# Kernel optimization log

Hardware: AMD Instinct MI355X
Metric: run time of the kernel (lower is better)

Reference implementation:

```python
import jax, jax.numpy as jnp
import numpy as np

B, N, C, H, BS = 4, 4096, 1024, 16, 64
E = C // H          # head dim = 64
EPS = 1e-3

def setup_inputs() -> dict:
    key = jax.random.key(0)
    k0, k1, k2, k3 = jax.random.split(key, 4)
    x = jax.random.normal(k0, (B, N, C), jnp.float32)
    qkv_w = jax.random.normal(k1, (3 * C, C), jnp.float32) * 0.02
    proj_w = jax.random.normal(k2, (C, C), jnp.float32) * 0.02
    proj_b = jax.random.normal(k3, (C,), jnp.float32) * 0.02
    return {"x": x, "qkv_w": qkv_w, "proj_w": proj_w, "proj_b": proj_b}

def reference(x, qkv_w, proj_w, proj_b):
    b, n, c = x.shape
    h, e, bs = H, E, BS
    u = n // bs  # number of buckets
    # qkv projection (no bias), split to (B,H,N,e) per q/k/v
    qkv = (x @ qkv_w.T).reshape(b, n, 3, h, e).transpose(2, 0, 3, 1, 4)
    q, k, v = qkv[0], qkv[1], qkv[2]
    # feature maps: softmax(q) scaled, exp(k)
    q = jax.nn.softmax(q, axis=-1) * (e ** -0.5)
    k = jnp.exp(k)
    # bucket along sequence: (B,H,U,BS,e)
    b_q = q.reshape(b, h, u, bs, e)
    b_k = k.reshape(b, h, u, bs, e)
    b_v = v.reshape(b, h, u, bs, e)
    # per-bucket k sums and inter-bucket cumulative sums
    b_k_cumsum = jnp.cumsum(b_k.sum(axis=-2), axis=-2)            # (B,H,U,e)
    context = jnp.einsum('bhund,bhune->bhude', b_k, b_v)          # (B,H,U,e,e)
    context = jnp.cumsum(context, axis=2)
    # exclusive shift by one bucket (bucket_size > 1 path in original)
    context = jnp.concatenate(
        [jnp.zeros_like(context[:, :, :1]), context[:, :, :-1]], axis=2)
    b_k_cumsum = jnp.concatenate(
        [jnp.zeros_like(b_k_cumsum[:, :, :1]), b_k_cumsum[:, :, :-1]], axis=2)
    # normalizer, clamped from below at eps
    D_inv = 1.0 / jnp.maximum(
        jnp.einsum('bhud,bhund->bhun', b_k_cumsum, b_q), EPS)
    attn = jnp.einsum('bhund,bhude,bhun->bhune', b_q, context, D_inv)
    out = attn.reshape(b, h, n, e).transpose(0, 2, 1, 3).reshape(b, n, c)
    # output projection (dropouts are identity at eval)
    return out @ proj_w.T + proj_b
```

## Files before the change

kernel.cpp:

```cpp
#include <hip/hip_runtime.h>
#include <stdint.h>


typedef unsigned short u16;
typedef u16   u16x4  __attribute__((ext_vector_type(4)));
typedef u16   u16x8  __attribute__((ext_vector_type(8)));
typedef float f32x4  __attribute__((ext_vector_type(4)));
typedef float float4v __attribute__((ext_vector_type(4)));
typedef __bf16 bf16x8 __attribute__((ext_vector_type(8)));

__device__ __forceinline__ u16 f2bf(float f) {
  return __builtin_bit_cast(u16, (__bf16)f);
}
__device__ __forceinline__ float bf2f(u16 h) {
  return (float)__builtin_bit_cast(__bf16, h);
}

__global__ __launch_bounds__(256) void cvt_f32_to_bf16(
    const float* __restrict__ in, u16* __restrict__ out, int n4) {
  int i = blockIdx.x * 256 + threadIdx.x;
  if (i >= n4) return;
  float4v v = reinterpret_cast<const float4v*>(in)[i];
  u16x4 o;
  o.x = f2bf(v.x); o.y = f2bf(v.y); o.z = f2bf(v.z); o.w = f2bf(v.w);
  reinterpret_cast<u16x4*>(out)[i] = o;
}

template <bool BF16_OUT>
__global__ __launch_bounds__(256, 2) void gemm_bt(
    const u16* __restrict__ A,
    const u16* __restrict__ B,
    const float* __restrict__ bias,
    void* __restrict__ Cv,
    int M, int N, int K) {
  __shared__ u16 As[128 * 64];
  __shared__ u16 Bs[128 * 64];
  const int tid  = threadIdx.x;
  const int lane = tid & 63;
  const int wave = tid >> 6;
  const int wm = wave >> 1, wn = wave & 1;
  const int l15 = lane & 15, l4 = lane >> 4;
  const int ntn = N >> 7;
  const int cpx = gridDim.x >> 3;
  const int bid = (blockIdx.x & 7) * cpx + (blockIdx.x >> 3);
  const int bm = bid / ntn, bn = bid % ntn;

  f32x4 acc[4][4] = {};

  const u16* Ab = A + (size_t)(bm * 128) * K;
  const u16* Bb = B + (size_t)(bn * 128) * K;
  const int crow = tid >> 3;
  const int ccol = tid & 7;

  for (int kt = 0; kt < K; kt += 64) {
    u16x8 ra[4], rb[4];
#pragma unroll
    for (int j = 0; j < 4; ++j) {
      int row = crow + 32 * j;
      ra[j] = *reinterpret_cast<const u16x8*>(Ab + (size_t)row * K + kt + ccol * 8);
      rb[j] = *reinterpret_cast<const u16x8*>(Bb + (size_t)row * K + kt + ccol * 8);
    }
    __syncthreads();
#pragma unroll
    for (int j = 0; j < 4; ++j) {
      int row = crow + 32 * j;
      int off = row * 128 + ((ccol * 16) ^ ((row & 7) << 4));
      *reinterpret_cast<u16x8*>(reinterpret_cast<char*>(As) + off) = ra[j];
      *reinterpret_cast<u16x8*>(reinterpret_cast<char*>(Bs) + off) = rb[j];
    }
    __syncthreads();
#pragma unroll
    for (int kk = 0; kk < 2; ++kk) {
      const int cb = kk * 64 + l4 * 16;
      bf16x8 af[4], bfr[4];
#pragma unroll
      for (int mi = 0; mi < 4; ++mi) {
        int row = wm * 64 + mi * 16 + l15;
        af[mi] = *reinterpret_cast<const bf16x8*>(
            reinterpret_cast<const char*>(As) + row * 128 + (cb ^ ((row & 7) << 4)));
      }
#pragma unroll
      for (int ni = 0; ni < 4; ++ni) {
        int row = wn * 64 + ni * 16 + l15;
        bfr[ni] = *reinterpret_cast<const bf16x8*>(
            reinterpret_cast<const char*>(Bs) + row * 128 + (cb ^ ((row & 7) << 4)));
      }
#pragma unroll
      for (int mi = 0; mi < 4; ++mi)
#pragma unroll
        for (int ni = 0; ni < 4; ++ni)
          acc[mi][ni] = __builtin_amdgcn_mfma_f32_16x16x32_bf16(
              af[mi], bfr[ni], acc[mi][ni], 0, 0, 0);
    }
  }

  const int row0 = bm * 128 + wm * 64 + l4 * 4;
  const int col0 = bn * 128 + wn * 64 + l15;
  if constexpr (BF16_OUT) {
    u16* C = (u16*)Cv;
#pragma unroll
    for (int mi = 0; mi < 4; ++mi)
#pragma unroll
      for (int i = 0; i < 4; ++i) {
        size_t r = (size_t)(row0 + mi * 16 + i) * N;
#pragma unroll
        for (int ni = 0; ni < 4; ++ni)
          C[r + col0 + ni * 16] = f2bf(acc[mi][ni][i]);
      }
  } else {
    float* C = (float*)Cv;
    float bv[4];
#pragma unroll
    for (int ni = 0; ni < 4; ++ni) bv[ni] = bias[col0 + ni * 16];
#pragma unroll
    for (int mi = 0; mi < 4; ++mi)
#pragma unroll
      for (int i = 0; i < 4; ++i) {
        size_t r = (size_t)(row0 + mi * 16 + i) * N;
#pragma unroll
        for (int ni = 0; ni < 4; ++ni)
          C[r + col0 + ni * 16] = acc[mi][ni][i] + bv[ni];
      }
  }
}

__global__ __launch_bounds__(256) void featuremap_ctx(
    const u16* __restrict__ qkv,
    u16* __restrict__ Q, u16* __restrict__ ctxb, float* __restrict__ ksum) {
  const int bid = blockIdx.x;
  const int u = bid & 63;
  const int bh = bid >> 6;
  const int b = bh >> 4, h = bh & 15;
  const int tid = threadIdx.x, lane = tid & 63, wave = tid >> 6;
  const int l15 = lane & 15, l4 = lane >> 4;
  __shared__ float ts[64][65];
  __shared__ u16 KtL[64][72];
  __shared__ u16 VtL[64][72];
  __shared__ float dp[64][4];

  const size_t mrow  = (size_t)b * 4096 + u * 64;
  const size_t obase = (size_t)bid * 4096;

#pragma unroll 1
  for (int r = 0; r < 16; ++r) {
    int n = wave * 16 + r;
    float v = bf2f(qkv[(mrow + n) * 3072 + h * 64 + lane]);
    float mx = v;
#pragma unroll
    for (int o = 32; o; o >>= 1) mx = fmaxf(mx, __shfl_xor(mx, o));
    float ex = __expf(v - mx);
    float sm = ex;
#pragma unroll
    for (int o = 32; o; o >>= 1) sm += __shfl_xor(sm, o);
    Q[obase + n * 64 + lane] = f2bf(ex / sm * 0.125f);
  }

  {
    int n = tid >> 2, c = tid & 3;
    const u16* kp = qkv + (mrow + n) * 3072 + 1024 + h * 64 + c * 16;
#pragma unroll
    for (int j = 0; j < 16; ++j) ts[n][c * 16 + j] = __expf(bf2f(kp[j]));
  }
  __syncthreads();
  {
    int d = tid >> 2, c = tid & 3;
    u16x8 o0, o1;
#pragma unroll
    for (int j = 0; j < 8; ++j) o0[j] = f2bf(ts[c * 16 + j][d]);
#pragma unroll
    for (int j = 0; j < 8; ++j) o1[j] = f2bf(ts[c * 16 + 8 + j][d]);
    *reinterpret_cast<u16x8*>(&KtL[d][c * 16])     = o0;
    *reinterpret_cast<u16x8*>(&KtL[d][c * 16 + 8]) = o1;
  }
  __syncthreads();
  {
    int d = tid & 63, q = tid >> 6;
    float a = 0.f;
#pragma unroll
    for (int j = 0; j < 16; ++j) a += bf2f(KtL[d][q * 16 + j]);
    dp[d][q] = a;
  }
  {
    int n = tid >> 2, c = tid & 3;
    const u16* vp = qkv + (mrow + n) * 3072 + 2048 + h * 64 + c * 16;
#pragma unroll
    for (int j = 0; j < 16; ++j) ts[n][c * 16 + j] = bf2f(vp[j]);
  }
  __syncthreads();
  if (tid < 64)
    ksum[obase / 64 + tid] = dp[tid][0] + dp[tid][1] + dp[tid][2] + dp[tid][3];
  {
    int e = tid >> 2, c = tid & 3;
    u16x8 o0, o1;
#pragma unroll
    for (int j = 0; j < 8; ++j) o0[j] = f2bf(ts[c * 16 + j][e]);
#pragma unroll
    for (int j = 0; j < 8; ++j) o1[j] = f2bf(ts[c * 16 + 8 + j][e]);
    *reinterpret_cast<u16x8*>(&VtL[e][c * 16])     = o0;
    *reinterpret_cast<u16x8*>(&VtL[e][c * 16 + 8]) = o1;
  }
  __syncthreads();

  f32x4 acc[4] = {};
#pragma unroll
  for (int kk = 0; kk < 2; ++kk) {
    bf16x8 av = *reinterpret_cast<const bf16x8*>(&VtL[wave * 16 + l15][kk * 32 + l4 * 8]);
#pragma unroll
    for (int ni = 0; ni < 4; ++ni) {
      bf16x8 bk = *reinterpret_cast<const bf16x8*>(&KtL[ni * 16 + l15][kk * 32 + l4 * 8]);
      acc[ni] = __builtin_amdgcn_mfma_f32_16x16x32_bf16(av, bk, acc[ni], 0, 0, 0);
    }
  }
  u16* cb = ctxb + obase;
#pragma unroll
  for (int ni = 0; ni < 4; ++ni)
#pragma unroll
    for (int i = 0; i < 4; ++i)
      cb[(wave * 16 + l4 * 4 + i) * 64 + ni * 16 + l15] = f2bf(acc[ni][i]);
}

__global__ __launch_bounds__(256) void scanctx(
    u16* __restrict__ ctxb, float* __restrict__ ksum) {
  const int bh = blockIdx.x >> 2, c = blockIdx.x & 3;
  const int tid = threadIdx.x;
  u16* p = ctxb + (size_t)bh * 64 * 4096 + c * 1024 + tid * 4;
  float* kp = ksum + (size_t)bh * 64 * 64 + tid;
  const bool dok = (c == 0) && (tid < 64);

  float r0 = 0.f, r1 = 0.f, r2 = 0.f, r3 = 0.f, runk = 0.f;
#define LC(i) (*reinterpret_cast<const u16x4*>(p + (size_t)(i) * 4096))
#define LK(i) (dok ? kp[(size_t)(i) * 64] : 0.f)
  u16x4 c0 = LC(0), c1 = LC(1), c2 = LC(2), c3 = LC(3);
  float k0 = LK(0), k1 = LK(1), k2 = LK(2), k3 = LK(3);
  for (int u = 0; u < 64; u += 4) {
    const int i4 = u + 4 < 64 ? u + 4 : 63, i5 = u + 5 < 64 ? u + 5 : 63;
    const int i6 = u + 6 < 64 ? u + 6 : 63, i7 = u + 7 < 64 ? u + 7 : 63;
    u16x4 n0 = LC(i4), n1 = LC(i5), n2 = LC(i6), n3 = LC(i7);
    float m0 = LK(i4), m1 = LK(i5), m2 = LK(i6), m3 = LK(i7);
#define STEP(idx, cv, kv)                                                  \
    {                                                                      \
      u16x4 o;                                                             \
      o.x = f2bf(r0); o.y = f2bf(r1); o.z = f2bf(r2); o.w = f2bf(r3);      \
      *reinterpret_cast<u16x4*>(p + (size_t)(idx) * 4096) = o;             \
      if (dok) kp[(size_t)(idx) * 64] = runk;                              \
      r0 += bf2f(cv.x); r1 += bf2f(cv.y); r2 += bf2f(cv.z);                \
      r3 += bf2f(cv.w); runk += kv;                                        \
    }
    STEP(u, c0, k0) STEP(u + 1, c1, k1) STEP(u + 2, c2, k2) STEP(u + 3, c3, k3)
#undef STEP
    c0 = n0; c1 = n1; c2 = n2; c3 = n3;
    k0 = m0; k1 = m1; k2 = m2; k3 = m3;
  }
#undef LC
#undef LK
}

__global__ __launch_bounds__(256) void apply(
    const u16* __restrict__ Q, const u16* __restrict__ ctxc,
    const float* __restrict__ kcum, u16* __restrict__ AT) {
  const int bid = blockIdx.x;
  const int u = bid & 63, bh = bid >> 6, b = bh >> 4, h = bh & 15;
  const int tid = threadIdx.x, lane = tid & 63, wave = tid >> 6;
  const int l15 = lane & 15, l4 = lane >> 4;
  __shared__ float kc[64];
  __shared__ float dp[64][4];
  __shared__ float dinv[64];

  const size_t base = (size_t)bid * 4096;
  const u16* Qu = Q + base;
  if (tid < 64) kc[tid] = kcum[(size_t)bid * 64 + tid];
  __syncthreads();
  {
    int n = tid & 63, q = tid >> 6;
    const u16* qp = Qu + n * 64 + q * 16;
    float a = 0.f;
#pragma unroll
    for (int j = 0; j < 16; ++j) a += bf2f(qp[j]) * kc[q * 16 + j];
    dp[n][q] = a;
  }
  __syncthreads();
  if (tid < 64)
    dinv[tid] = 1.f / fmaxf(dp[tid][0] + dp[tid][1] + dp[tid][2] + dp[tid][3], 1e-3f);
  __syncthreads();

  f32x4 acc[4] = {};
  const u16* Cu = ctxc + base;
#pragma unroll
  for (int kk = 0; kk < 2; ++kk) {
    bf16x8 aq = *reinterpret_cast<const bf16x8*>(Qu + (wave * 16 + l15) * 64 + kk * 32 + l4 * 8);
#pragma unroll
    for (int ni = 0; ni < 4; ++ni) {
      bf16x8 bc = *reinterpret_cast<const bf16x8*>(Cu + (ni * 16 + l15) * 64 + kk * 32 + l4 * 8);
      acc[ni] = __builtin_amdgcn_mfma_f32_16x16x32_bf16(aq, bc, acc[ni], 0, 0, 0);
    }
  }
  const size_t orow = ((size_t)b * 4096 + u * 64 + wave * 16 + l4 * 4) * 1024 + h * 64;
#pragma unroll
  for (int i = 0; i < 4; ++i) {
    float di = dinv[wave * 16 + l4 * 4 + i];
#pragma unroll
    for (int ni = 0; ni < 4; ++ni)
      AT[orow + (size_t)i * 1024 + ni * 16 + l15] = f2bf(acc[ni][i] * di);
  }
}

extern "C" void kernel_launch(void* const* d_in, const int* in_sizes, int n_in,
                              void* d_out, int out_size, void* d_ws, size_t ws_size,
                              hipStream_t stream) {
  (void)in_sizes; (void)n_in; (void)out_size; (void)ws_size;
  const float* x      = (const float*)d_in[0];
  const float* qkv_w  = (const float*)d_in[1];
  const float* proj_w = (const float*)d_in[2];
  const float* proj_b = (const float*)d_in[3];
  float* out = (float*)d_out;

  char* ws = (char*)d_ws;
  u16* xb    = (u16*)(ws);
  u16* wq    = (u16*)(ws + 33554432);
  u16* wp    = (u16*)(ws + 39845888);
  u16* qkv   = (u16*)(ws + 41943040);
  u16* Qf    = (u16*)(ws + 142606336);
  u16* ctxb  = (u16*)(ws + 176160768);
  float* ksum = (float*)(ws + 209715200);
  u16* AT    = qkv;

  cvt_f32_to_bf16<<<dim3(16384), dim3(256), 0, stream>>>(x, xb, 16777216 / 4);
  cvt_f32_to_bf16<<<dim3(3072),  dim3(256), 0, stream>>>(qkv_w, wq, 3145728 / 4);
  cvt_f32_to_bf16<<<dim3(1024),  dim3(256), 0, stream>>>(proj_w, wp, 1048576 / 4);

  gemm_bt<true ><<<dim3(128 * 24), dim3(256), 0, stream>>>(xb, wq, nullptr, qkv,
                                                           16384, 3072, 1024);
  featuremap_ctx<<<dim3(4096), dim3(256), 0, stream>>>(qkv, Qf, ctxb, ksum);
  scanctx<<<dim3(256), dim3(256), 0, stream>>>(ctxb, ksum);
  apply<<<dim3(4096), dim3(256), 0, stream>>>(Qf, ctxb, ksum, AT);
  gemm_bt<false><<<dim3(128 * 8), dim3(256), 0, stream>>>(AT, wp, proj_b, out,
                                                          16384, 1024, 1024);
}
```

Measured before the change: 291.6 us.

## Replace GEMM with 256x256-tile double-buffered direct-to-LDS pipelined kernel

```diff
diff --git a/kernel.cpp b/kernel.cpp
--- a/kernel.cpp
+++ b/kernel.cpp
@@ -3,6 +3,7 @@
 
 
 typedef unsigned short u16;
+typedef unsigned int u32;
 typedef u16   u16x4  __attribute__((ext_vector_type(4)));
 typedef u16   u16x8  __attribute__((ext_vector_type(8)));
 typedef float f32x4  __attribute__((ext_vector_type(4)));
@@ -14,6 +15,12 @@
 }
 __device__ __forceinline__ float bf2f(u16 h) {
   return (float)__builtin_bit_cast(__bf16, h);
+}
+
+__device__ __forceinline__ void stage16(const u16* g, u16* l) {
+  __builtin_amdgcn_global_load_lds(
+      (const __attribute__((address_space(1))) u32*)g,
+      (__attribute__((address_space(3))) u32*)l, 16, 0, 0);
 }
 
 __global__ __launch_bounds__(256) void cvt_f32_to_bf16(
@@ -27,79 +34,116 @@
 }
 
 template <bool BF16_OUT>
-__global__ __launch_bounds__(256, 2) void gemm_bt(
+__global__ __launch_bounds__(512, 2) void gemm256(
     const u16* __restrict__ A,
     const u16* __restrict__ B,
     const float* __restrict__ bias,
     void* __restrict__ Cv,
-    int M, int N, int K) {
-  __shared__ u16 As[128 * 64];
-  __shared__ u16 Bs[128 * 64];
-  const int tid  = threadIdx.x;
-  const int lane = tid & 63;
-  const int wave = tid >> 6;
-  const int wm = wave >> 1, wn = wave & 1;
+    int N, int K, int NT) {
+  __shared__ u16 As[2][2][256][32];
+  __shared__ u16 Bs[2][2][256][32];
+  const int tid = threadIdx.x, lane = tid & 63, wave = tid >> 6;
+  const int wm = wave >> 2, wn = wave & 3;
   const int l15 = lane & 15, l4 = lane >> 4;
-  const int ntn = N >> 7;
+  const int ntn = N >> 8;
   const int cpx = gridDim.x >> 3;
   const int bid = (blockIdx.x & 7) * cpx + (blockIdx.x >> 3);
   const int bm = bid / ntn, bn = bid % ntn;
 
-  f32x4 acc[4][4] = {};
-
-  const u16* Ab = A + (size_t)(bm * 128) * K;
-  const u16* Bb = B + (size_t)(bn * 128) * K;
-  const int crow = tid >> 3;
-  const int ccol = tid & 7;
-
-  for (int kt = 0; kt < K; kt += 64) {
-    u16x8 ra[4], rb[4];
-#pragma unroll
-    for (int j = 0; j < 4; ++j) {
-      int row = crow + 32 * j;
-      ra[j] = *reinterpret_cast<const u16x8*>(Ab + (size_t)row * K + kt + ccol * 8);
-      rb[j] = *reinterpret_cast<const u16x8*>(Bb + (size_t)row * K + kt + ccol * 8);
-    }
-    __syncthreads();
-#pragma unroll
-    for (int j = 0; j < 4; ++j) {
-      int row = crow + 32 * j;
-      int off = row * 128 + ((ccol * 16) ^ ((row & 7) << 4));
-      *reinterpret_cast<u16x8*>(reinterpret_cast<char*>(As) + off) = ra[j];
-      *reinterpret_cast<u16x8*>(reinterpret_cast<char*>(Bs) + off) = rb[j];
-    }
-    __syncthreads();
-#pragma unroll
-    for (int kk = 0; kk < 2; ++kk) {
-      const int cb = kk * 64 + l4 * 16;
-      bf16x8 af[4], bfr[4];
-#pragma unroll
-      for (int mi = 0; mi < 4; ++mi) {
-        int row = wm * 64 + mi * 16 + l15;
-        af[mi] = *reinterpret_cast<const bf16x8*>(
-            reinterpret_cast<const char*>(As) + row * 128 + (cb ^ ((row & 7) << 4)));
-      }
-#pragma unroll
-      for (int ni = 0; ni < 4; ++ni) {
-        int row = wn * 64 + ni * 16 + l15;
-        bfr[ni] = *reinterpret_cast<const bf16x8*>(
-            reinterpret_cast<const char*>(Bs) + row * 128 + (cb ^ ((row & 7) << 4)));
-      }
-#pragma unroll
-      for (int mi = 0; mi < 4; ++mi)
-#pragma unroll
-        for (int ni = 0; ni < 4; ++ni)
-          acc[mi][ni] = __builtin_amdgcn_mfma_f32_16x16x32_bf16(
-              af[mi], bfr[ni], acc[mi][ni], 0, 0, 0);
-    }
-  }
-
-  const int row0 = bm * 128 + wm * 64 + l4 * 4;
-  const int col0 = bn * 128 + wn * 64 + l15;
+  const int srow = tid >> 2;
+  const int gsl8 = ((tid & 3) ^ ((tid >> 3) & 3)) * 8;
+  const u16* Ag = A + (size_t)(bm * 256 + srow) * K + gsl8;
+  const u16* Bg = B + (size_t)(bn * 256 + srow) * K + gsl8;
+  const size_t rj = (size_t)128 * K;
+
+  const int slotr = (l4 ^ ((l15 >> 1) & 3)) * 8;
+
+  f32x4 acc[8][4] = {};
+  bf16x8 a0, a1, a2, a3, b0, b1, b2, b3;
+
+#define STG(P, buf, kh, kt)                                        \
+  { const u16* g_ = P##g + (kt) + (kh) * 32;                       \
+    stage16(g_,      &P##s[buf][kh][wave * 16][0]);                \
+    stage16(g_ + rj, &P##s[buf][kh][128 + wave * 16][0]); }
+
+#define LDA(kk, mh)                                                \
+  { const u16* p_ = &As[cur][kk][wm * 128 + (mh) * 64 + l15][0] + slotr; \
+    a0 = *(const bf16x8*)(p_);                                     \
+    a1 = *(const bf16x8*)(p_ + 512);                               \
+    a2 = *(const bf16x8*)(p_ + 1024);                              \
+    a3 = *(const bf16x8*)(p_ + 1536); }
+
+#define LDB(kk)                                                    \
+  { const u16* p_ = &Bs[cur][kk][wn * 64 + l15][0] + slotr;        \
+    b0 = *(const bf16x8*)(p_);                                     \
+    b1 = *(const bf16x8*)(p_ + 512);                               \
+    b2 = *(const bf16x8*)(p_ + 1024);                              \
+    b3 = *(const bf16x8*)(p_ + 1536); }
+
+#define MM(x, y, z) z = __builtin_amdgcn_mfma_f32_16x16x32_bf16(x, y, z, 0, 0, 0)
+#define MFMA16(mb)                                                 \
+  __builtin_amdgcn_s_setprio(1);                                   \
+  MM(a0, b0, acc[(mb) + 0][0]); MM(a0, b1, acc[(mb) + 0][1]);      \
+  MM(a0, b2, acc[(mb) + 0][2]); MM(a0, b3, acc[(mb) + 0][3]);      \
+  MM(a1, b0, acc[(mb) + 1][0]); MM(a1, b1, acc[(mb) + 1][1]);      \
+  MM(a1, b2, acc[(mb) + 1][2]); MM(a1, b3, acc[(mb) + 1][3]);      \
+  MM(a2, b0, acc[(mb) + 2][0]); MM(a2, b1, acc[(mb) + 2][1]);      \
+  MM(a2, b2, acc[(mb) + 2][2]); MM(a2, b3, acc[(mb) + 2][3]);      \
+  MM(a3, b0, acc[(mb) + 3][0]); MM(a3, b1, acc[(mb) + 3][1]);      \
+  MM(a3, b2, acc[(mb) + 3][2]); MM(a3, b3, acc[(mb) + 3][3]);      \
+  __builtin_amdgcn_s_setprio(0);
+
+#define BARF()                                                     \
+  { asm volatile("" ::: "memory");                                 \
+    __builtin_amdgcn_s_barrier();                                  \
+    asm volatile("" ::: "memory"); }
+
+  STG(A, 0, 0, 0) STG(B, 0, 0, 0) STG(A, 0, 1, 0) STG(B, 0, 1, 0)
+  asm volatile("s_waitcnt vmcnt(0)" ::: "memory");
+  __builtin_amdgcn_s_barrier();
+  asm volatile("" ::: "memory");
+
+  for (int t = 0; t < NT; ++t) {
+    const int cur = t & 1, nxt = cur ^ 1;
+    const int ktn = (t + 1) << 6;
+    const bool pre = (t + 1 < NT);
+    LDB(0) LDA(0, 0)
+    if (pre) STG(A, nxt, 0, ktn)
+    BARF()
+    MFMA16(0)
+    BARF()
+    LDA(0, 1)
+    if (pre) STG(B, nxt, 0, ktn)
+    BARF()
+    MFMA16(4)
+    if (pre) { asm volatile("s_waitcnt vmcnt(4)" ::: "memory"); }
+    else     { asm volatile("s_waitcnt vmcnt(0)" ::: "memory"); }
+    BARF()
+    LDB(1) LDA(1, 0)
+    if (pre) STG(A, nxt, 1, ktn)
+    BARF()
+    MFMA16(0)
+    BARF()
+    LDA(1, 1)
+    if (pre) STG(B, nxt, 1, ktn)
+    BARF()
+    MFMA16(4)
+    if (pre) { asm volatile("s_waitcnt vmcnt(4)" ::: "memory"); }
+    BARF()
+  }
+#undef STG
+#undef LDA
+#undef LDB
+#undef MM
+#undef MFMA16
+#undef BARF
+
+  const int row0 = bm * 256 + wm * 128 + l4 * 4;
+  const int col0 = bn * 256 + wn * 64 + l15;
   if constexpr (BF16_OUT) {
     u16* C = (u16*)Cv;
 #pragma unroll
-    for (int mi = 0; mi < 4; ++mi)
+    for (int mi = 0; mi < 8; ++mi)
 #pragma unroll
       for (int i = 0; i < 4; ++i) {
         size_t r = (size_t)(row0 + mi * 16 + i) * N;
@@ -113,7 +157,7 @@
 #pragma unroll
     for (int ni = 0; ni < 4; ++ni) bv[ni] = bias[col0 + ni * 16];
 #pragma unroll
-    for (int mi = 0; mi < 4; ++mi)
+    for (int mi = 0; mi < 8; ++mi)
 #pragma unroll
       for (int i = 0; i < 4; ++i) {
         size_t r = (size_t)(row0 + mi * 16 + i) * N;
@@ -328,11 +372,11 @@
   cvt_f32_to_bf16<<<dim3(3072),  dim3(256), 0, stream>>>(qkv_w, wq, 3145728 / 4);
   cvt_f32_to_bf16<<<dim3(1024),  dim3(256), 0, stream>>>(proj_w, wp, 1048576 / 4);
 
-  gemm_bt<true ><<<dim3(128 * 24), dim3(256), 0, stream>>>(xb, wq, nullptr, qkv,
-                                                           16384, 3072, 1024);
+  gemm256<true ><<<dim3(64 * 12), dim3(512), 0, stream>>>(xb, wq, nullptr, qkv,
+                                                          3072, 1024, 16);
   featuremap_ctx<<<dim3(4096), dim3(256), 0, stream>>>(qkv, Qf, ctxb, ksum);
   scanctx<<<dim3(256), dim3(256), 0, stream>>>(ctxb, ksum);
   apply<<<dim3(4096), dim3(256), 0, stream>>>(Qf, ctxb, ksum, AT);
-  gemm_bt<false><<<dim3(128 * 8), dim3(256), 0, stream>>>(AT, wp, proj_b, out,
-                                                          16384, 1024, 1024);
-}
+  gemm256<false><<<dim3(64 * 4), dim3(512), 0, stream>>>(AT, wp, proj_b, out,
+                                                         1024, 1024, 16);
+}
```

New measurement: 286.8 us. Within noise of the previous version (-1.6%).
